# Kernel tuning notes

Measured on AMD Instinct MI355X. Metric: run time of the kernel, lower is better.

The kernel has to match this reference:

```python
import jax, jax.numpy as jnp
import numpy as np

EPS = 1e-5

def _layernorm(x, w, b):
    mu = jnp.mean(x, axis=-1, keepdims=True)
    var = jnp.mean(jnp.square(x - mu), axis=-1, keepdims=True)
    return (x - mu) * jax.lax.rsqrt(var + EPS) * w + b

def setup_inputs() -> dict:
    key = jax.random.key(0)
    ks = jax.random.split(key, 9)
    N, P_DIM, D = 16384, 3072, 1024
    patches = jax.random.normal(ks[0], (N, P_DIM), dtype=jnp.float32)
    bbox_coords = jax.random.uniform(ks[1], (N, 4), dtype=jnp.float32)
    ln1_w = jnp.ones((P_DIM,), dtype=jnp.float32)
    ln1_b = jnp.zeros((P_DIM,), dtype=jnp.float32)
    W_patch = jax.random.normal(ks[2], (D, P_DIM), dtype=jnp.float32) * (P_DIM ** -0.5)
    class_emb = jax.random.normal(ks[3], (1, 1, D), dtype=jnp.float32)
    W_pos = jax.random.normal(ks[4], (D, 4), dtype=jnp.float32) * 0.5
    b_pos = jax.random.normal(ks[5], (D,), dtype=jnp.float32) * 0.02
    class_pos = jax.random.normal(ks[6], (1, D), dtype=jnp.float32)
    return {"patches": patches, "bbox_coords": bbox_coords, "ln1_w": ln1_w,
            "ln1_b": ln1_b, "W_patch": W_patch, "class_emb": class_emb,
            "W_pos": W_pos, "b_pos": b_pos, "class_pos": class_pos}

def reference(patches, bbox_coords, ln1_w, ln1_b, W_patch, class_emb, W_pos, b_pos, class_pos):
    # Batched equivalent of the per-patch loop: LayerNorm -> Linear (no bias).
    # NOTE: torch code computes patch_norm2 but appends the PRE-norm2 embedding,
    # so norm2 is dead code and omitted here.
    x = _layernorm(patches, ln1_w, ln1_b)                      # [N, patch_dim]
    patch_embeds = jnp.einsum('np,dp->nd', x, W_patch)          # [N, D]
    embeddings = jnp.concatenate([class_emb, patch_embeds[None]], axis=1)  # [1, N+1, D]
    pos = jnp.einsum('nc,dc->nd', bbox_coords, W_pos) + b_pos   # [N, D]
    pos_full = jnp.concatenate([class_pos[None], pos[None]], axis=1)       # [1, N+1, D]
    return embeddings + pos_full
```

## Files before the change

kernel.cpp:

```cpp
#include <hip/hip_runtime.h>

typedef unsigned short u16;
typedef __attribute__((ext_vector_type(8))) short bf16x8;
typedef __attribute__((ext_vector_type(4))) float f32x4;

#define AS1C(p) ((const __attribute__((address_space(1))) void*)(p))
#define AS3(p)  ((__attribute__((address_space(3))) void*)(p))

#define CFENCE() asm volatile("" ::: "memory")

__device__ __forceinline__ u16 f2bf(float f) {
    unsigned u = __float_as_uint(f);
    u += 0x7fffu + ((u >> 16) & 1u);
    return (u16)(u >> 16);
}

__global__ __launch_bounds__(256) void prep_kernel(
    const float* __restrict__ x, const float* __restrict__ w,
    const float* __restrict__ b, const float* __restrict__ Wp,
    const float* __restrict__ ce, const float* __restrict__ cp,
    u16* __restrict__ A, u16* __restrict__ Wb, float* __restrict__ out,
    int N, int D, int K)
{
    const int blk = blockIdx.x;
    const int t = threadIdx.x;

    if (blk < N) {
        const float* xr = x + (size_t)blk * K;
        float4 v[3];
#pragma unroll
        for (int i = 0; i < 3; ++i)
            v[i] = *(const float4*)&xr[(i * 256 + t) * 4];

        float s = 0.f;
#pragma unroll
        for (int i = 0; i < 3; ++i) s += v[i].x + v[i].y + v[i].z + v[i].w;
#pragma unroll
        for (int off = 32; off; off >>= 1) s += __shfl_down(s, off);

        __shared__ float red[8];
        const int wid = t >> 6, lane = t & 63;
        if (lane == 0) red[wid] = s;
        __syncthreads();
        const float mu = (red[0] + red[1] + red[2] + red[3]) * (1.0f / 3072.0f);

        float sq = 0.f;
#pragma unroll
        for (int i = 0; i < 3; ++i) {
            float dx = v[i].x - mu, dy = v[i].y - mu, dz = v[i].z - mu, dw = v[i].w - mu;
            sq += dx * dx + dy * dy + dz * dz + dw * dw;
        }
#pragma unroll
        for (int off = 32; off; off >>= 1) sq += __shfl_down(sq, off);
        if (lane == 0) red[4 + wid] = sq;
        __syncthreads();
        const float var = (red[4] + red[5] + red[6] + red[7]) * (1.0f / 3072.0f);
        const float inv = rsqrtf(var + 1e-5f);

#pragma unroll
        for (int i = 0; i < 3; ++i) {
            const int j = (i * 256 + t) * 4;
            const float4 wv = *(const float4*)&w[j];
            const float4 bv = *(const float4*)&b[j];
            ushort4 o;
            o.x = f2bf((v[i].x - mu) * inv * wv.x + bv.x);
            o.y = f2bf((v[i].y - mu) * inv * wv.y + bv.y);
            o.z = f2bf((v[i].z - mu) * inv * wv.z + bv.z);
            o.w = f2bf((v[i].w - mu) * inv * wv.w + bv.w);
            *(ushort4*)&A[(size_t)blk * K + j] = o;
        }
    } else if (blk < N + D) {
        const int row = blk - N;
        const float* wr = Wp + (size_t)row * K;
#pragma unroll
        for (int i = 0; i < 3; ++i) {
            const int j = (i * 256 + t) * 4;
            const float4 v = *(const float4*)&wr[j];
            ushort4 o;
            o.x = f2bf(v.x); o.y = f2bf(v.y); o.z = f2bf(v.z); o.w = f2bf(v.w);
            *(ushort4*)&Wb[(size_t)row * K + j] = o;
        }
    } else {
#pragma unroll
        for (int i = 0; i < 4; ++i) {
            const int j = i * 256 + t;
            out[j] = ce[j] + cp[j];
        }
    }
}

#define STG_A(BUFOFS, R0, T_) \
    __builtin_amdgcn_global_load_lds(AS1C(aS + (size_t)(R0) * 3072 + (T_) * 64), \
                                     AS3(dA + (BUFOFS) + (R0) * 128), 16, 0, 0)
#define STG_B(BUFOFS, R0, T_) \
    __builtin_amdgcn_global_load_lds(AS1C(bS + (size_t)(R0) * 3072 + (T_) * 64), \
                                     AS3(dB + (BUFOFS) + (R0) * 128), 16, 0, 0)

#define MFMA16(d, a, b) d = __builtin_amdgcn_mfma_f32_16x16x32_bf16(a, b, d, 0, 0, 0)

#define PH16(BUF, MH, KH, STG, WT) do {                                           \
    const char* Ab = L + (BUF) + aRowBase + (MH) * 8192;                          \
    const char* Bb = L + (BUF) + bRowBase;                                        \
    const int ck = (KH) ? ckh1 : ckh0;                                            \
    bf16x8 a0 = *(const bf16x8*)(Ab + 0 * 2048 + ck);                             \
    bf16x8 a1 = *(const bf16x8*)(Ab + 1 * 2048 + ck);                             \
    bf16x8 a2 = *(const bf16x8*)(Ab + 2 * 2048 + ck);                             \
    bf16x8 a3 = *(const bf16x8*)(Ab + 3 * 2048 + ck);                             \
    bf16x8 b0 = *(const bf16x8*)(Bb + 0 * 2048 + ck);                             \
    bf16x8 b1 = *(const bf16x8*)(Bb + 1 * 2048 + ck);                             \
    bf16x8 b2 = *(const bf16x8*)(Bb + 2 * 2048 + ck);                             \
    bf16x8 b3 = *(const bf16x8*)(Bb + 3 * 2048 + ck);                             \
    STG;                                                                          \
    __builtin_amdgcn_s_barrier();                                                 \
    asm volatile("s_waitcnt lgkmcnt(0)" ::: "memory");                            \
    __builtin_amdgcn_s_setprio(1);                                                \
    MFMA16(acc[(MH)*4+0][0], a0, b0); MFMA16(acc[(MH)*4+0][1], a0, b1);           \
    MFMA16(acc[(MH)*4+0][2], a0, b2); MFMA16(acc[(MH)*4+0][3], a0, b3);           \
    MFMA16(acc[(MH)*4+1][0], a1, b0); MFMA16(acc[(MH)*4+1][1], a1, b1);           \
    MFMA16(acc[(MH)*4+1][2], a1, b2); MFMA16(acc[(MH)*4+1][3], a1, b3);           \
    MFMA16(acc[(MH)*4+2][0], a2, b0); MFMA16(acc[(MH)*4+2][1], a2, b1);           \
    MFMA16(acc[(MH)*4+2][2], a2, b2); MFMA16(acc[(MH)*4+2][3], a2, b3);           \
    MFMA16(acc[(MH)*4+3][0], a3, b0); MFMA16(acc[(MH)*4+3][1], a3, b1);           \
    MFMA16(acc[(MH)*4+3][2], a3, b2); MFMA16(acc[(MH)*4+3][3], a3, b3);           \
    __builtin_amdgcn_s_setprio(0);                                                \
    WT;                                                                           \
    __builtin_amdgcn_s_barrier();                                                 \
    CFENCE();                                                                     \
} while (0)

__global__ __launch_bounds__(512, 2) void gemm_256_cnt_kernel(
    const u16* __restrict__ A, const u16* __restrict__ W,
    const float* __restrict__ bbox, const float* __restrict__ Wpos,
    const float* __restrict__ bpos, float* __restrict__ out,
    int D)
{
    __shared__ __align__(16) char lds[131072];
    const char* L = (const char*)lds;
    const int K = 3072;
    const int NK = 48;

    const int bid = blockIdx.x;
    const int swb = (bid & 7) * 32 + (bid >> 3);
    const int bx = swb & 3;
    const int by = swb >> 2;
    const int brow = by * 256;
    const int bcol = bx * 256;

    const int t = threadIdx.x;
    const int wid = t >> 6, lane = t & 63;
    const int wm = wid >> 2;
    const int wn = wid & 3;
    const int fr = lane & 15;
    const int kq16 = ((lane >> 4) & 3) * 16;
    const int xorb = (fr & 7) << 4;
    const int aRowBase = (wm * 128 + fr) * 128;
    const int bRowBase = 32768 + (wn * 64 + fr) * 128;
    const int ckh0 = (0  + kq16) ^ xorb;
    const int ckh1 = (64 + kq16) ^ xorb;

    const int srow = t >> 3;
    const int scol = ((t & 7) ^ ((t >> 3) & 7)) * 8;
    const u16* aS = A + (size_t)(brow + srow) * K + scol;
    const u16* bS = W + (size_t)(bcol + srow) * K + scol;
    char* dA = (char*)lds + t * 16;
    char* dB = (char*)lds + 32768 + t * 16;

    f32x4 acc[8][4] = {};

    STG_B(0, 0, 0);   STG_B(0, 64, 0);  STG_B(0, 128, 0); STG_B(0, 192, 0);
    STG_A(0, 0, 0);   STG_A(0, 128, 0); STG_A(0, 64, 0);  STG_A(0, 192, 0);
    asm volatile("s_waitcnt vmcnt(0)" ::: "memory");
    __builtin_amdgcn_s_barrier();
    CFENCE();

    for (int T = 0; T < NK; T += 2) {
        const bool more = (T + 2) < NK;
        PH16(0, 0, 0, { STG_B(65536, 0, T + 1); STG_B(65536, 64, T + 1); }, ((void)0));
        PH16(0, 0, 1, { STG_B(65536, 128, T + 1); STG_B(65536, 192, T + 1); },
             { asm volatile("s_waitcnt vmcnt(4)" ::: "memory"); });
        PH16(0, 1, 0, { STG_A(65536, 0, T + 1); STG_A(65536, 128, T + 1); }, ((void)0));
        PH16(0, 1, 1, { STG_A(65536, 64, T + 1); STG_A(65536, 192, T + 1); },
             { asm volatile("s_waitcnt vmcnt(2)" ::: "memory"); });
        PH16(65536, 0, 0, { if (more) { STG_B(0, 0, T + 2); STG_B(0, 64, T + 2); } }, ((void)0));
        PH16(65536, 0, 1, { if (more) { STG_B(0, 128, T + 2); STG_B(0, 192, T + 2); } },
             { if (more) asm volatile("s_waitcnt vmcnt(4)" ::: "memory");
               else      asm volatile("s_waitcnt vmcnt(0)" ::: "memory"); });
        PH16(65536, 1, 0, { if (more) { STG_A(0, 0, T + 2); STG_A(0, 128, T + 2); } }, ((void)0));
        PH16(65536, 1, 1, { if (more) { STG_A(0, 64, T + 2); STG_A(0, 192, T + 2); } },
             { if (more) asm volatile("s_waitcnt vmcnt(2)" ::: "memory"); });
    }

    float* Lf = (float*)lds;
    const int r4 = ((lane >> 4) & 3) * 4;
    const int cg = bcol + lane * 4;

    float4 wpv[4];
    float bpv[4];
#pragma unroll
    for (int j = 0; j < 4; ++j) {
        wpv[j] = *(const float4*)&Wpos[(cg + j) * 4];
        bpv[j] = bpos[cg + j];
    }

#pragma unroll
    for (int c = 0; c < 4; ++c) {
        __builtin_amdgcn_s_barrier();
        CFENCE();
#pragma unroll
        for (int q = 0; q < 2; ++q) {
#pragma unroll
            for (int n = 0; n < 4; ++n) {
                const f32x4 v = acc[c * 2 + q][n];
                const int col = wn * 64 + n * 16 + fr;
#pragma unroll
                for (int r = 0; r < 4; ++r)
                    Lf[(wm * 32 + q * 16 + r4 + r) * 256 + col] = v[r];
            }
        }
        __builtin_amdgcn_s_barrier();
        CFENCE();
#pragma unroll
        for (int i = 0; i < 8; ++i) {
            const int lrow = wid + 8 * i;
            const int gr = brow + (lrow >> 5) * 128 + c * 32 + (lrow & 31);
            const float4 v = *(const float4*)&Lf[lrow * 256 + lane * 4];
            const float4 bb = *(const float4*)&bbox[(size_t)gr * 4];
            float4 o;
            o.x = v.x + bpv[0] + bb.x * wpv[0].x + bb.y * wpv[0].y + bb.z * wpv[0].z + bb.w * wpv[0].w;
            o.y = v.y + bpv[1] + bb.x * wpv[1].x + bb.y * wpv[1].y + bb.z * wpv[1].z + bb.w * wpv[1].w;
            o.z = v.z + bpv[2] + bb.x * wpv[2].x + bb.y * wpv[2].y + bb.z * wpv[2].z + bb.w * wpv[2].w;
            o.w = v.w + bpv[3] + bb.x * wpv[3].x + bb.y * wpv[3].y + bb.z * wpv[3].z + bb.w * wpv[3].w;
            *(float4*)&out[(size_t)(gr + 1) * D + cg] = o;
        }
    }
}

extern "C" void kernel_launch(void* const* d_in, const int* in_sizes, int n_in,
                              void* d_out, int out_size, void* d_ws, size_t ws_size,
                              hipStream_t stream)
{
    const float* patches   = (const float*)d_in[0];
    const float* bbox      = (const float*)d_in[1];
    const float* ln1_w     = (const float*)d_in[2];
    const float* ln1_b     = (const float*)d_in[3];
    const float* W_patch   = (const float*)d_in[4];
    const float* class_emb = (const float*)d_in[5];
    const float* W_pos     = (const float*)d_in[6];
    const float* b_pos     = (const float*)d_in[7];
    const float* class_pos = (const float*)d_in[8];
    float* out = (float*)d_out;

    const int N = in_sizes[1] / 4;
    const int K = in_sizes[2];
    const int D = in_sizes[7];

    u16* Abf = (u16*)d_ws;
    u16* Wbf = Abf + (size_t)N * K;

    prep_kernel<<<N + D + 1, 256, 0, stream>>>(patches, ln1_w, ln1_b, W_patch,
                                               class_emb, class_pos, Abf, Wbf, out,
                                               N, D, K);

    const int nblk = (N / 256) * (D / 256);
    gemm_256_cnt_kernel<<<nblk, 512, 0, stream>>>(Abf, Wbf, bbox, W_pos, b_pos, out, D);
}
```

Measured before the change: 156.1 us.

## Restructure GEMM main loop with register-reused B fragments and fine-grained LDS waits

Rewrites the bf16 GEMM inner loop so each K-tile runs in two barrier-separated halves instead of four phases with a barrier each. B fragments are loaded once per k-half and reused across both M halves. LDS reads for the next MFMA group are issued early, and staged lgkmcnt waits let MFMAs start before all fragments arrive. The aim is fewer barriers and better overlap of LDS reads with MFMA work, at the cost of more live VGPRs (extra fragment registers) and fragile hand-counted waitcnt values.

```diff
diff --git a/kernel.cpp b/kernel.cpp
--- a/kernel.cpp
+++ b/kernel.cpp
@@ -98,37 +98,43 @@
 
 #define MFMA16(d, a, b) d = __builtin_amdgcn_mfma_f32_16x16x32_bf16(a, b, d, 0, 0, 0)
 
-#define PH16(BUF, MH, KH, STG, WT) do {                                           \
-    const char* Ab = L + (BUF) + aRowBase + (MH) * 8192;                          \
-    const char* Bb = L + (BUF) + bRowBase;                                        \
-    const int ck = (KH) ? ckh1 : ckh0;                                            \
-    bf16x8 a0 = *(const bf16x8*)(Ab + 0 * 2048 + ck);                             \
-    bf16x8 a1 = *(const bf16x8*)(Ab + 1 * 2048 + ck);                             \
-    bf16x8 a2 = *(const bf16x8*)(Ab + 2 * 2048 + ck);                             \
-    bf16x8 a3 = *(const bf16x8*)(Ab + 3 * 2048 + ck);                             \
-    bf16x8 b0 = *(const bf16x8*)(Bb + 0 * 2048 + ck);                             \
-    bf16x8 b1 = *(const bf16x8*)(Bb + 1 * 2048 + ck);                             \
-    bf16x8 b2 = *(const bf16x8*)(Bb + 2 * 2048 + ck);                             \
-    bf16x8 b3 = *(const bf16x8*)(Bb + 3 * 2048 + ck);                             \
-    STG;                                                                          \
-    __builtin_amdgcn_s_barrier();                                                 \
-    asm volatile("s_waitcnt lgkmcnt(0)" ::: "memory");                            \
+#define LGKM_(N_) asm volatile("s_waitcnt lgkmcnt(" #N_ ")" ::: "memory"); \
+                  __builtin_amdgcn_sched_barrier(0)
+#define LGKM(N_) LGKM_(N_)
+
+#define BARRIER() { __builtin_amdgcn_s_barrier(); CFENCE(); }
+#define VMW_(N_) asm volatile("s_waitcnt vmcnt(" #N_ ")" ::: "memory")
+#define VMW(N_) VMW_(N_)
+
+#define RD_B(BUF, CK, H0, H1, H2, H3) \
+    H0 = *(const bf16x8*)(L + (BUF) + bRowBase + 0 * 2048 + (CK)); \
+    H1 = *(const bf16x8*)(L + (BUF) + bRowBase + 1 * 2048 + (CK)); \
+    H2 = *(const bf16x8*)(L + (BUF) + bRowBase + 2 * 2048 + (CK)); \
+    H3 = *(const bf16x8*)(L + (BUF) + bRowBase + 3 * 2048 + (CK))
+
+#define RD_A(BUF, MH, CK, P0, P1, P2, P3) \
+    P0 = *(const bf16x8*)(L + (BUF) + aRowBase + (MH) * 8192 + 0 * 2048 + (CK)); \
+    P1 = *(const bf16x8*)(L + (BUF) + aRowBase + (MH) * 8192 + 1 * 2048 + (CK)); \
+    P2 = *(const bf16x8*)(L + (BUF) + aRowBase + (MH) * 8192 + 2 * 2048 + (CK)); \
+    P3 = *(const bf16x8*)(L + (BUF) + aRowBase + (MH) * 8192 + 3 * 2048 + (CK))
+
+#define LADR(MH, A0, A1, A2, A3, H0, H1, H2, H3, W3, W2, W1, W0)                  \
     __builtin_amdgcn_s_setprio(1);                                                \
-    MFMA16(acc[(MH)*4+0][0], a0, b0); MFMA16(acc[(MH)*4+0][1], a0, b1);           \
-    MFMA16(acc[(MH)*4+0][2], a0, b2); MFMA16(acc[(MH)*4+0][3], a0, b3);           \
-    MFMA16(acc[(MH)*4+1][0], a1, b0); MFMA16(acc[(MH)*4+1][1], a1, b1);           \
-    MFMA16(acc[(MH)*4+1][2], a1, b2); MFMA16(acc[(MH)*4+1][3], a1, b3);           \
-    MFMA16(acc[(MH)*4+2][0], a2, b0); MFMA16(acc[(MH)*4+2][1], a2, b1);           \
-    MFMA16(acc[(MH)*4+2][2], a2, b2); MFMA16(acc[(MH)*4+2][3], a2, b3);           \
-    MFMA16(acc[(MH)*4+3][0], a3, b0); MFMA16(acc[(MH)*4+3][1], a3, b1);           \
-    MFMA16(acc[(MH)*4+3][2], a3, b2); MFMA16(acc[(MH)*4+3][3], a3, b3);           \
-    __builtin_amdgcn_s_setprio(0);                                                \
-    WT;                                                                           \
-    __builtin_amdgcn_s_barrier();                                                 \
-    CFENCE();                                                                     \
-} while (0)
-
-__global__ __launch_bounds__(512, 2) void gemm_256_cnt_kernel(
+    LGKM(W3);                                                                     \
+    MFMA16(acc[(MH)*4+0][0], A0, H0); MFMA16(acc[(MH)*4+0][1], A0, H1);           \
+    MFMA16(acc[(MH)*4+0][2], A0, H2); MFMA16(acc[(MH)*4+0][3], A0, H3);           \
+    LGKM(W2);                                                                     \
+    MFMA16(acc[(MH)*4+1][0], A1, H0); MFMA16(acc[(MH)*4+1][1], A1, H1);           \
+    MFMA16(acc[(MH)*4+1][2], A1, H2); MFMA16(acc[(MH)*4+1][3], A1, H3);           \
+    LGKM(W1);                                                                     \
+    MFMA16(acc[(MH)*4+2][0], A2, H0); MFMA16(acc[(MH)*4+2][1], A2, H1);           \
+    MFMA16(acc[(MH)*4+2][2], A2, H2); MFMA16(acc[(MH)*4+2][3], A2, H3);           \
+    LGKM(W0);                                                                     \
+    MFMA16(acc[(MH)*4+3][0], A3, H0); MFMA16(acc[(MH)*4+3][1], A3, H1);           \
+    MFMA16(acc[(MH)*4+3][2], A3, H2); MFMA16(acc[(MH)*4+3][3], A3, H3);           \
+    __builtin_amdgcn_s_setprio(0)
+
+__global__ __launch_bounds__(512, 2) void gemm_256_r22_kernel(
     const u16* __restrict__ A, const u16* __restrict__ W,
     const float* __restrict__ bbox, const float* __restrict__ Wpos,
     const float* __restrict__ bpos, float* __restrict__ out,
@@ -166,28 +172,58 @@
     char* dB = (char*)lds + 32768 + t * 16;
 
     f32x4 acc[8][4] = {};
+    bf16x8 hbA0, hbA1, hbA2, hbA3;
+    bf16x8 hbB0, hbB1, hbB2, hbB3;
+    bf16x8 q0, q1, q2, q3;
+    bf16x8 r0, r1, r2, r3;
+    bf16x8 s0, s1, s2, s3;
+    bf16x8 u0, u1, u2, u3;
 
     STG_B(0, 0, 0);   STG_B(0, 64, 0);  STG_B(0, 128, 0); STG_B(0, 192, 0);
     STG_A(0, 0, 0);   STG_A(0, 128, 0); STG_A(0, 64, 0);  STG_A(0, 192, 0);
-    asm volatile("s_waitcnt vmcnt(0)" ::: "memory");
-    __builtin_amdgcn_s_barrier();
-    CFENCE();
+    VMW(0);
+    BARRIER();
 
     for (int T = 0; T < NK; T += 2) {
         const bool more = (T + 2) < NK;
-        PH16(0, 0, 0, { STG_B(65536, 0, T + 1); STG_B(65536, 64, T + 1); }, ((void)0));
-        PH16(0, 0, 1, { STG_B(65536, 128, T + 1); STG_B(65536, 192, T + 1); },
-             { asm volatile("s_waitcnt vmcnt(4)" ::: "memory"); });
-        PH16(0, 1, 0, { STG_A(65536, 0, T + 1); STG_A(65536, 128, T + 1); }, ((void)0));
-        PH16(0, 1, 1, { STG_A(65536, 64, T + 1); STG_A(65536, 192, T + 1); },
-             { asm volatile("s_waitcnt vmcnt(2)" ::: "memory"); });
-        PH16(65536, 0, 0, { if (more) { STG_B(0, 0, T + 2); STG_B(0, 64, T + 2); } }, ((void)0));
-        PH16(65536, 0, 1, { if (more) { STG_B(0, 128, T + 2); STG_B(0, 192, T + 2); } },
-             { if (more) asm volatile("s_waitcnt vmcnt(4)" ::: "memory");
-               else      asm volatile("s_waitcnt vmcnt(0)" ::: "memory"); });
-        PH16(65536, 1, 0, { if (more) { STG_A(0, 0, T + 2); STG_A(0, 128, T + 2); } }, ((void)0));
-        PH16(65536, 1, 1, { if (more) { STG_A(0, 64, T + 2); STG_A(0, 192, T + 2); } },
-             { if (more) asm volatile("s_waitcnt vmcnt(2)" ::: "memory"); });
+
+        RD_B(0, ckh0, hbA0, hbA1, hbA2, hbA3);
+        RD_A(0, 0, ckh0, q0, q1, q2, q3);
+        STG_B(65536, 0, T + 1); STG_B(65536, 64, T + 1);
+        LADR(0, q0, q1, q2, q3, hbA0, hbA1, hbA2, hbA3, 3, 2, 1, 0);
+        VMW(2);
+        BARRIER();
+        RD_A(0, 1, ckh0, r0, r1, r2, r3);
+        RD_B(0, ckh1, hbB0, hbB1, hbB2, hbB3);
+        RD_A(0, 0, ckh1, s0, s1, s2, s3);
+        STG_B(65536, 128, T + 1); STG_B(65536, 192, T + 1);
+        LADR(1, r0, r1, r2, r3, hbA0, hbA1, hbA2, hbA3, 11, 10, 9, 8);
+        RD_A(0, 1, ckh1, u0, u1, u2, u3);
+        STG_A(65536, 0, T + 1); STG_A(65536, 128, T + 1);
+        LADR(0, s0, s1, s2, s3, hbB0, hbB1, hbB2, hbB3, 7, 6, 5, 4);
+        STG_A(65536, 64, T + 1); STG_A(65536, 192, T + 1);
+        LADR(1, u0, u1, u2, u3, hbB0, hbB1, hbB2, hbB3, 3, 2, 1, 0);
+        VMW(2);
+        BARRIER();
+
+        RD_B(65536, ckh0, hbA0, hbA1, hbA2, hbA3);
+        RD_A(65536, 0, ckh0, q0, q1, q2, q3);
+        if (more) { STG_B(0, 0, T + 2); STG_B(0, 64, T + 2); }
+        LADR(0, q0, q1, q2, q3, hbA0, hbA1, hbA2, hbA3, 3, 2, 1, 0);
+        if (more) { VMW(2); } else { VMW(0); }
+        BARRIER();
+        RD_A(65536, 1, ckh0, r0, r1, r2, r3);
+        RD_B(65536, ckh1, hbB0, hbB1, hbB2, hbB3);
+        RD_A(65536, 0, ckh1, s0, s1, s2, s3);
+        if (more) { STG_B(0, 128, T + 2); STG_B(0, 192, T + 2); }
+        LADR(1, r0, r1, r2, r3, hbA0, hbA1, hbA2, hbA3, 11, 10, 9, 8);
+        RD_A(65536, 1, ckh1, u0, u1, u2, u3);
+        if (more) { STG_A(0, 0, T + 2); STG_A(0, 128, T + 2); }
+        LADR(0, s0, s1, s2, s3, hbB0, hbB1, hbB2, hbB3, 7, 6, 5, 4);
+        if (more) { STG_A(0, 64, T + 2); STG_A(0, 192, T + 2); }
+        LADR(1, u0, u1, u2, u3, hbB0, hbB1, hbB2, hbB3, 3, 2, 1, 0);
+        if (more) { VMW(2); }
+        BARRIER();
     }
 
     float* Lf = (float*)lds;
@@ -204,8 +240,7 @@
 
 #pragma unroll
     for (int c = 0; c < 4; ++c) {
-        __builtin_amdgcn_s_barrier();
-        CFENCE();
+        __syncthreads();
 #pragma unroll
         for (int q = 0; q < 2; ++q) {
 #pragma unroll
@@ -217,8 +252,7 @@
                     Lf[(wm * 32 + q * 16 + r4 + r) * 256 + col] = v[r];
             }
         }
-        __builtin_amdgcn_s_barrier();
-        CFENCE();
+        __syncthreads();
 #pragma unroll
         for (int i = 0; i < 8; ++i) {
             const int lrow = wid + 8 * i;
@@ -262,5 +296,5 @@
                                                N, D, K);
 
     const int nblk = (N / 256) * (D / 256);
-    gemm_256_cnt_kernel<<<nblk, 512, 0, stream>>>(Abf, Wbf, bbox, W_pos, b_pos, out, D);
+    gemm_256_r22_kernel<<<nblk, 512, 0, stream>>>(Abf, Wbf, bbox, W_pos, b_pos, out, D);
 }
```

Measured after the change: 241.9 us. +55.0%, slower.
